# Kernel optimization log

Hardware: AMD Instinct MI355X
Metric: run time of the kernel (lower is better)

Reference implementation:

```python
import jax, jax.numpy as jnp
import numpy as np

N = 50000   # nodes
E = 800000  # edges
G = 64      # graphs in batch
D = 128     # joint_embed_dim
H = D // 2  # 64
NEG_SLOPE = 0.2


def _segment_softmax(logits, seg, n):
    m = jax.ops.segment_max(logits, seg, num_segments=n)
    m = jnp.where(jnp.isfinite(m), m, 0.0)
    e = jnp.exp(logits - m[seg])
    s = jax.ops.segment_sum(e, seg, num_segments=n)
    return e / (s[seg] + 1e-16)


def _gat_conv(x, src, dst, W, a_src, a_dst, b, n):
    # PyG GATConv, heads=1, add_self_loops=True
    loops = jnp.arange(n, dtype=src.dtype)
    s = jnp.concatenate([src, loops])
    d = jnp.concatenate([dst, loops])
    h = x @ W                                   # [n, out]
    alpha_s = h @ a_src                         # [n]
    alpha_d = h @ a_dst
    logit = jax.nn.leaky_relu(alpha_s[s] + alpha_d[d], NEG_SLOPE)  # [E+n]
    alpha = _segment_softmax(logit, d, n)
    out = jax.ops.segment_sum(h[s] * alpha[:, None], d, num_segments=n)
    return out + b


def _edge_conv(x, src, dst, We1, be1, We2, be2, n):
    # PyG EdgeConv: max_j nn(cat[x_i, x_j - x_i])
    xi = x[dst]
    xj = x[src]
    feats = jnp.concatenate([xi, xj - xi], axis=1)     # [E, 2*H]
    m = jax.nn.relu(feats @ We1 + be1)
    m = jax.nn.relu(m @ We2 + be2)
    out = jax.ops.segment_max(m, dst, num_segments=n)
    return jnp.where(jnp.isfinite(out), out, 0.0)


def setup_inputs() -> dict:
    key = jax.random.key(0)
    ks = jax.random.split(key, 24)
    x = jax.random.normal(ks[0], (N, 3), dtype=jnp.float32)
    edge_index = jax.random.randint(ks[1], (2, E), 0, N, dtype=jnp.int64)
    batch_ids = jnp.sort(jax.random.randint(ks[2], (N,), 0, G, dtype=jnp.int64))

    def w(k, shape, fan_in):
        return jax.random.normal(k, shape, dtype=jnp.float32) * (1.0 / np.sqrt(fan_in))

    inp = {
        "x": x, "edge_index": edge_index, "batch_ids": batch_ids,
        # GATConv1: 3 -> 64
        "W1": w(ks[3], (3, H), 3), "a1s": w(ks[4], (H,), H), "a1d": w(ks[5], (H,), H), "b1": jnp.zeros((H,), jnp.float32),
        # GATConv2: 64 -> 64
        "W2": w(ks[6], (H, H), H), "a2s": w(ks[7], (H,), H), "a2d": w(ks[8], (H,), H), "b2": jnp.zeros((H,), jnp.float32),
        # GATConv3: 128 -> 128
        "W3": w(ks[9], (D, D), D), "a3s": w(ks[10], (D,), D), "a3d": w(ks[11], (D,), D), "b3": jnp.zeros((D,), jnp.float32),
        # EdgeConv nn: 128 -> 128 -> 128
        "We1": w(ks[12], (D, D), D), "be1": jnp.zeros((D,), jnp.float32),
        "We2": w(ks[13], (D, D), D), "be2": jnp.zeros((D,), jnp.float32),
        # MLP: 256 -> 128 -> 128
        "Wm1": w(ks[14], (2 * D, D), 2 * D), "bm1": jnp.zeros((D,), jnp.float32),
        "Wm2": w(ks[15], (D, D), D), "bm2": jnp.zeros((D,), jnp.float32),
    }
    return inp


def reference(x, edge_index, batch_ids,
              W1, a1s, a1d, b1, W2, a2s, a2d, b2, W3, a3s, a3d, b3,
              We1, be1, We2, be2, Wm1, bm1, Wm2, bm2):
    src, dst = edge_index[0], edge_index[1]
    n = x.shape[0]
    # conv1 + relu (dropout is identity in eval)
    h = jax.nn.relu(_gat_conv(x, src, dst, W1, a1s, a1d, b1, n))
    # conv2 + elu
    h = jax.nn.elu(_gat_conv(h, src, dst, W2, a2s, a2d, b2, n))
    # edge_conv: 64 -> 128
    h = _edge_conv(h, src, dst, We1, be1, We2, be2, n)
    # conv3 + relu
    h = jax.nn.relu(_gat_conv(h, src, dst, W3, a3s, a3d, b3, n))
    # global mean / max pool over graphs
    sums = jax.ops.segment_sum(h, batch_ids, num_segments=G)
    cnts = jax.ops.segment_sum(jnp.ones((n, 1), h.dtype), batch_ids, num_segments=G)
    mean_pool = sums / jnp.maximum(cnts, 1.0)
    max_pool = jax.ops.segment_max(h, batch_ids, num_segments=G)
    max_pool = jnp.where(jnp.isfinite(max_pool), max_pool, 0.0)
    z = jnp.concatenate([mean_pool, max_pool], axis=1)    # [G, 256]
    z = jax.nn.relu(z @ Wm1 + bm1)
    z = jax.nn.relu(z @ Wm2 + bm2)
    norm = jnp.linalg.norm(z, axis=1, keepdims=True)
    return z / jnp.maximum(norm, 1e-12)
```

## Files before the change

### kernel.cpp

```cpp
#include <hip/hip_runtime.h>
#include <hip/hip_bf16.h>
#include <math.h>


typedef __attribute__((ext_vector_type(4))) float f32x4;
typedef __attribute__((ext_vector_type(8))) short bf16x8;
typedef __attribute__((ext_vector_type(8))) ushort u16x8;
typedef short s16x2 __attribute__((ext_vector_type(2)));

__device__ __forceinline__ float wave_sum(float v) {
#pragma unroll
  for (int o = 32; o > 0; o >>= 1) v += __shfl_xor(v, o, 64);
  return v;
}
__device__ __forceinline__ float wave_max(float v) {
#pragma unroll
  for (int o = 32; o > 0; o >>= 1) v = fmaxf(v, __shfl_xor(v, o, 64));
  return v;
}
__device__ __forceinline__ float half_sum(float v) {
#pragma unroll
  for (int o = 16; o > 0; o >>= 1) v += __shfl_xor(v, o, 64);
  return v;
}
__device__ __forceinline__ float half_max(float v) {
#pragma unroll
  for (int o = 16; o > 0; o >>= 1) v = fmaxf(v, __shfl_xor(v, o, 64));
  return v;
}
__device__ __forceinline__ float lrelu(float x) { return x >= 0.f ? x : 0.2f * x; }
__device__ __forceinline__ ushort f2bf(float f) {
  union { float f; unsigned u; } v; v.f = f;
  unsigned r = (v.u + 0x7fff + ((v.u >> 16) & 1)) >> 16;
  return (ushort)r;
}
__device__ __forceinline__ float bf2f(ushort u) {
  union { unsigned u; float f; } v; v.u = ((unsigned)u) << 16;
  return v.f;
}
__device__ __forceinline__ float bflo(unsigned v) { return __uint_as_float(v << 16); }
__device__ __forceinline__ float bfhi(unsigned v) { return __uint_as_float(v & 0xffff0000u); }
__device__ __forceinline__ unsigned pack2bf(float a, float b) {
  __hip_bfloat162 h = __float22bfloat162_rn(make_float2(a, b));
  union { __hip_bfloat162 h; unsigned u; } cv;
  cv.h = h;
  return cv.u;
}
__device__ __forceinline__ unsigned bfadd2_relu(unsigned a, unsigned b) {
  union { unsigned u; __hip_bfloat162 h; s16x2 s; } ua, ub, ur;
  ua.u = a;
  ub.u = b;
  ur.h = __hadd2(ua.h, ub.h);
  s16x2 z = (s16x2)0;
  ur.s = __builtin_elementwise_max(ur.s, z);
  return ur.u;
}


__global__ void count_kernel(const int* __restrict__ ei, int* __restrict__ deg, int E) {
  int e = blockIdx.x * 256 + threadIdx.x;
  if (e < E) atomicAdd(&deg[ei[E + e]], 1);
}

__global__ void scan_local(const int* __restrict__ deg, int* __restrict__ off,
                           int* __restrict__ bsum, int n) {
  __shared__ int buf[256];
  int i = blockIdx.x * 256 + threadIdx.x;
  int v = (i < n) ? deg[i] : 0;
  buf[threadIdx.x] = v;
  __syncthreads();
  int incl = v;
  for (int o = 1; o < 256; o <<= 1) {
    int t = (threadIdx.x >= o) ? buf[threadIdx.x - o] : 0;
    __syncthreads();
    incl += t;
    buf[threadIdx.x] = incl;
    __syncthreads();
  }
  if (i < n) off[i] = incl - v;
  if (threadIdx.x == 255) bsum[blockIdx.x] = incl;
}

__global__ void scan_bsum(int* __restrict__ bsum, int nb) {
  __shared__ int buf[256];
  int v = (threadIdx.x < nb) ? bsum[threadIdx.x] : 0;
  buf[threadIdx.x] = v;
  __syncthreads();
  int incl = v;
  for (int o = 1; o < 256; o <<= 1) {
    int t = (threadIdx.x >= o) ? buf[threadIdx.x - o] : 0;
    __syncthreads();
    incl += t;
    buf[threadIdx.x] = incl;
    __syncthreads();
  }
  if (threadIdx.x < nb) bsum[threadIdx.x] = incl - v;
}

__global__ void scan_add(int* __restrict__ off, const int* __restrict__ bsum, int n, int total) {
  int i = blockIdx.x * 256 + threadIdx.x;
  if (i < n) off[i] += bsum[blockIdx.x];
  if (i == 0) off[n] = total;
}

__global__ void scatter_kernel(const int* __restrict__ ei, const int* __restrict__ off,
                               int* __restrict__ cursor, int* __restrict__ csr_src,
                               int* __restrict__ csr_dst, int E) {
  int e = blockIdx.x * 256 + threadIdx.x;
  if (e < E) {
    int d = ei[E + e];
    int pos = off[d] + atomicAdd(&cursor[d], 1);
    csr_src[pos] = ei[e];
    csr_dst[pos] = d;
  }
}


template <int IN, int OUT>
__global__ __launch_bounds__(256) void node_linear_kernel(
    const float* __restrict__ x, const float* __restrict__ W,
    const float* __restrict__ av_s, const float* __restrict__ av_d,
    ushort* __restrict__ hb, float* __restrict__ as_out, float* __restrict__ ad_out, int n) {
  constexpr int NC = OUT / 64;
  constexpr int NB = 4;
  __shared__ float Wl[IN * OUT];
  if constexpr ((IN * OUT) % 1024 == 0) {
    for (int i = threadIdx.x; i < IN * OUT / 4; i += 256)
      ((float4*)Wl)[i] = ((const float4*)W)[i];
  } else {
    for (int i = threadIdx.x; i < IN * OUT; i += 256) Wl[i] = W[i];
  }
  __syncthreads();
  const int wid = threadIdx.x >> 6, lane = threadIdx.x & 63;
  const int n0 = (blockIdx.x * 4 + wid) * NB;
  if (n0 >= n) return;
  float acc[NB][NC];
#pragma unroll
  for (int j = 0; j < NB; ++j)
#pragma unroll
    for (int c = 0; c < NC; ++c) acc[j][c] = 0.f;
  int nidx[NB];
#pragma unroll
  for (int j = 0; j < NB; ++j) nidx[j] = min(n0 + j, n - 1);

  if constexpr ((IN & 3) == 0) {
#pragma unroll 2
    for (int k = 0; k < IN; k += 4) {
      float4 xv[NB];
#pragma unroll
      for (int j = 0; j < NB; ++j) xv[j] = *(const float4*)&x[nidx[j] * IN + k];
#pragma unroll
      for (int kk = 0; kk < 4; ++kk) {
        float w[NC];
        if constexpr (NC == 2) {
          float2 wv = *(const float2*)&Wl[(k + kk) * OUT + 2 * lane];
          w[0] = wv.x;
          w[1] = wv.y;
        } else {
          w[0] = Wl[(k + kk) * OUT + lane];
        }
#pragma unroll
        for (int j = 0; j < NB; ++j) {
          float xk = (kk == 0) ? xv[j].x : (kk == 1) ? xv[j].y : (kk == 2) ? xv[j].z : xv[j].w;
#pragma unroll
          for (int c = 0; c < NC; ++c) acc[j][c] += xk * w[c];
        }
      }
    }
  } else {
    for (int k = 0; k < IN; ++k) {
      float w[NC];
#pragma unroll
      for (int c = 0; c < NC; ++c) w[c] = (NC == 2) ? Wl[k * OUT + 2 * lane + c] : Wl[k * OUT + lane];
#pragma unroll
      for (int j = 0; j < NB; ++j) {
        float xk = x[nidx[j] * IN + k];
#pragma unroll
        for (int c = 0; c < NC; ++c) acc[j][c] += xk * w[c];
      }
    }
  }

  float a_sv[NC], a_dv[NC];
#pragma unroll
  for (int c = 0; c < NC; ++c) {
    const int col = (NC == 2) ? 2 * lane + c : lane;
    a_sv[c] = av_s[col];
    a_dv[c] = av_d[col];
  }
#pragma unroll
  for (int j = 0; j < NB; ++j) {
    int node = n0 + j;
    if (node >= n) break;
    float ps = 0.f, pd = 0.f;
#pragma unroll
    for (int c = 0; c < NC; ++c) {
      ps += acc[j][c] * a_sv[c];
      pd += acc[j][c] * a_dv[c];
    }
    if constexpr (NC == 2) {
      unsigned pk = pack2bf(acc[j][0], acc[j][1]);
      *(unsigned*)&hb[(size_t)node * OUT + 2 * lane] = pk;
    } else {
      hb[(size_t)node * OUT + lane] = f2bf(acc[j][0]);
    }
    ps = wave_sum(ps);
    pd = wave_sum(pd);
    if (lane == 0) {
      as_out[node] = ps;
      ad_out[node] = pd;
    }
  }
}


template <int K>
__global__ void compute_wa(const float* __restrict__ W, const float* __restrict__ a_s,
                           const float* __restrict__ a_d, float* __restrict__ wa_s,
                           float* __restrict__ wa_d) {
  const int k = threadIdx.x;
  float s = 0.f, d = 0.f;
  for (int j = 0; j < K; ++j) {
    const float w = W[k * K + j];
    s += w * a_s[j];
    d += w * a_d[j];
  }
  wa_s[k] = s;
  wa_d[k] = d;
}


#define NT 64
#define M1S 136
#define M2S 132

__global__ __launch_bounds__(256, 4) void node_mfma_kernel(
    const float* __restrict__ x, const ushort* __restrict__ Wcm,
    const float* __restrict__ wa_s, const float* __restrict__ wa_d,
    ushort* __restrict__ hb, float* __restrict__ as_out, float* __restrict__ ad_out, int n) {
  __shared__ __align__(16) char smem[NT * M2S * 4];
  __shared__ float swa[128], swd[128];
  ushort* m1 = (ushort*)smem;
  float* m2 = (float*)smem;
  const int tid = threadIdx.x;
  const int lane = tid & 63, wid = tid >> 6;
  const int quad = lane >> 4, l16 = lane & 15;
  const int row = tid >> 2, c0 = (tid & 3) * 32;

  bf16x8 bfrag[2][4];
#pragma unroll
  for (int ct = 0; ct < 2; ++ct) {
    const int nn = wid * 32 + ct * 16 + l16;
#pragma unroll
    for (int ks = 0; ks < 4; ++ks)
      bfrag[ct][ks] = *(const bf16x8*)&Wcm[nn * 128 + ks * 32 + quad * 8];
  }
  if (tid < 128) {
    swa[tid] = wa_s[tid];
    swd[tid] = wa_d[tid];
  }
  __syncthreads();

  const int n0 = blockIdx.x * NT;
  const int node = min(n0 + row, n - 1);

  float ps = 0.f, pd = 0.f;
  {
    const float4* xp = (const float4*)&x[(size_t)node * 128 + c0];
#pragma unroll
    for (int i = 0; i < 4; ++i) {
      const float4 a = xp[2 * i], b = xp[2 * i + 1];
      const float4 wa0 = *(const float4*)&swa[c0 + 8 * i];
      const float4 wa1 = *(const float4*)&swa[c0 + 8 * i + 4];
      const float4 wd0 = *(const float4*)&swd[c0 + 8 * i];
      const float4 wd1 = *(const float4*)&swd[c0 + 8 * i + 4];
      ps += a.x * wa0.x + a.y * wa0.y + a.z * wa0.z + a.w * wa0.w
          + b.x * wa1.x + b.y * wa1.y + b.z * wa1.z + b.w * wa1.w;
      pd += a.x * wd0.x + a.y * wd0.y + a.z * wd0.z + a.w * wd0.w
          + b.x * wd1.x + b.y * wd1.y + b.z * wd1.z + b.w * wd1.w;
      uint4 rr;
      rr.x = pack2bf(a.x, a.y);
      rr.y = pack2bf(a.z, a.w);
      rr.z = pack2bf(b.x, b.y);
      rr.w = pack2bf(b.z, b.w);
      *((uint4*)&m1[row * M1S + c0] + i) = rr;
    }
  }
  ps += __shfl_xor(ps, 1, 64);
  ps += __shfl_xor(ps, 2, 64);
  pd += __shfl_xor(pd, 1, 64);
  pd += __shfl_xor(pd, 2, 64);
  if ((tid & 3) == 0 && n0 + row < n) {
    as_out[n0 + row] = ps;
    ad_out[n0 + row] = pd;
  }
  __syncthreads();

  f32x4 acc[4][2];
#pragma unroll
  for (int rt = 0; rt < 4; ++rt)
#pragma unroll
    for (int ct = 0; ct < 2; ++ct) acc[rt][ct] = (f32x4)0.f;
#pragma unroll
  for (int ks = 0; ks < 4; ++ks) {
    bf16x8 afr[4];
#pragma unroll
    for (int rt = 0; rt < 4; ++rt)
      afr[rt] = *(const bf16x8*)&m1[(rt * 16 + l16) * M1S + ks * 32 + quad * 8];
#pragma unroll
    for (int rt = 0; rt < 4; ++rt)
#pragma unroll
      for (int ct = 0; ct < 2; ++ct)
        acc[rt][ct] = __builtin_amdgcn_mfma_f32_16x16x32_bf16(afr[rt], bfrag[ct][ks],
                                                              acc[rt][ct], 0, 0, 0);
  }
  __syncthreads();

#pragma unroll
  for (int ct = 0; ct < 2; ++ct) {
    const int col = wid * 32 + ct * 16 + l16;
#pragma unroll
    for (int rt = 0; rt < 4; ++rt)
#pragma unroll
      for (int r = 0; r < 4; ++r) {
        const int rr2 = rt * 16 + quad * 4 + r;
        m2[rr2 * M2S + col] = acc[rt][ct][r];
      }
  }
  __syncthreads();

  unsigned* hbu = (unsigned*)hb;
#pragma unroll
  for (int i = 0; i < 16; ++i) {
    const int r = wid + 4 * i;
    if (n0 + r < n)
      hbu[(size_t)(n0 + r) * 64 + lane] =
          pack2bf(m2[r * M2S + 2 * lane], m2[r * M2S + 2 * lane + 1]);
  }
}


#define M1S64 72
#define M2S64 68

__global__ __launch_bounds__(256, 4) void node_mfma64_kernel(
    const float* __restrict__ x, const ushort* __restrict__ Wcm,
    const float* __restrict__ wa_s, const float* __restrict__ wa_d,
    ushort* __restrict__ hb, float* __restrict__ as_out, float* __restrict__ ad_out, int n) {
  __shared__ __align__(16) char smem[NT * M2S64 * 4];
  __shared__ float swa[64], swd[64];
  ushort* m1 = (ushort*)smem;
  float* m2 = (float*)smem;
  const int tid = threadIdx.x;
  const int lane = tid & 63, wid = tid >> 6;
  const int quad = lane >> 4, l16 = lane & 15;
  const int row = tid >> 2, c0 = (tid & 3) * 16;

  bf16x8 bfrag[2];
#pragma unroll
  for (int ks = 0; ks < 2; ++ks)
    bfrag[ks] = *(const bf16x8*)&Wcm[(wid * 16 + l16) * 64 + ks * 32 + quad * 8];
  if (tid < 64) {
    swa[tid] = wa_s[tid];
    swd[tid] = wa_d[tid];
  }
  __syncthreads();

  const int n0 = blockIdx.x * NT;
  const int node = min(n0 + row, n - 1);

  float ps = 0.f, pd = 0.f;
  {
    const float4* xp = (const float4*)&x[(size_t)node * 64 + c0];
#pragma unroll
    for (int i = 0; i < 2; ++i) {
      const float4 a = xp[2 * i], b = xp[2 * i + 1];
      const float4 wa0 = *(const float4*)&swa[c0 + 8 * i];
      const float4 wa1 = *(const float4*)&swa[c0 + 8 * i + 4];
      const float4 wd0 = *(const float4*)&swd[c0 + 8 * i];
      const float4 wd1 = *(const float4*)&swd[c0 + 8 * i + 4];
      ps += a.x * wa0.x + a.y * wa0.y + a.z * wa0.z + a.w * wa0.w
          + b.x * wa1.x + b.y * wa1.y + b.z * wa1.z + b.w * wa1.w;
      pd += a.x * wd0.x + a.y * wd0.y + a.z * wd0.z + a.w * wd0.w
          + b.x * wd1.x + b.y * wd1.y + b.z * wd1.z + b.w * wd1.w;
      uint4 rr;
      rr.x = pack2bf(a.x, a.y);
      rr.y = pack2bf(a.z, a.w);
      rr.z = pack2bf(b.x, b.y);
      rr.w = pack2bf(b.z, b.w);
      *((uint4*)&m1[row * M1S64 + c0] + i) = rr;
    }
  }
  ps += __shfl_xor(ps, 1, 64);
  ps += __shfl_xor(ps, 2, 64);
  pd += __shfl_xor(pd, 1, 64);
  pd += __shfl_xor(pd, 2, 64);
  if ((tid & 3) == 0 && n0 + row < n) {
    as_out[n0 + row] = ps;
    ad_out[n0 + row] = pd;
  }
  __syncthreads();

  f32x4 acc[4];
#pragma unroll
  for (int rt = 0; rt < 4; ++rt) acc[rt] = (f32x4)0.f;
#pragma unroll
  for (int ks = 0; ks < 2; ++ks) {
    bf16x8 afr[4];
#pragma unroll
    for (int rt = 0; rt < 4; ++rt)
      afr[rt] = *(const bf16x8*)&m1[(rt * 16 + l16) * M1S64 + ks * 32 + quad * 8];
#pragma unroll
    for (int rt = 0; rt < 4; ++rt)
      acc[rt] = __builtin_amdgcn_mfma_f32_16x16x32_bf16(afr[rt], bfrag[ks], acc[rt], 0, 0, 0);
  }
  __syncthreads();

  {
    const int col = wid * 16 + l16;
#pragma unroll
    for (int rt = 0; rt < 4; ++rt)
#pragma unroll
      for (int r = 0; r < 4; ++r) {
        const int rr2 = rt * 16 + quad * 4 + r;
        m2[rr2 * M2S64 + col] = acc[rt][r];
      }
  }
  __syncthreads();

  unsigned* hbu = (unsigned*)hb;
#pragma unroll
  for (int i = 0; i < 8; ++i) {
    const int r = wid * 2 + (lane >> 5) + 8 * i;
    const int j = lane & 31;
    if (n0 + r < n)
      hbu[(size_t)(n0 + r) * 32 + j] =
          pack2bf(m2[r * M2S64 + 2 * j], m2[r * M2S64 + 2 * j + 1]);
  }
}


template <int OUT, int ACT>
__global__ __launch_bounds__(256) void gat_agg_kernel(
    const ushort* __restrict__ h, const float* __restrict__ as_, const float* __restrict__ ad_,
    const float* __restrict__ bias, const int* __restrict__ off, const int* __restrict__ csr_src,
    float* __restrict__ out, int n) {
  constexpr int NC = OUT / 64;
  __shared__ float wbuf[4][64];
  __shared__ int sbuf[4][64];
  const int wid = threadIdx.x >> 6, lane = threadIdx.x & 63;
  const int d = blockIdx.x * 4 + wid;
  if (d >= n) return;
  const int s0 = off[d], s1 = off[d + 1];
  const float ad = ad_[d];
  const float l_self = lrelu(as_[d] + ad);
  unsigned selfv = 0;
  ushort selfu = 0;
  if constexpr (NC == 2)
    selfv = *(const unsigned*)&h[(size_t)d * OUT + 2 * lane];
  else
    selfu = h[(size_t)d * OUT + lane];

  float m = l_self;
  float esum_l = 0.f;
  float acc[NC];
#pragma unroll
  for (int c = 0; c < NC; ++c) acc[c] = 0.f;

  for (int base = s0; base < s1; base += 64) {
    const int cnt = min(64, s1 - base);
    const int idx = base + lane;
    float l = -3.0e38f;
    int s_l = 0;
    if (idx < s1) {
      s_l = csr_src[idx];
      l = lrelu(as_[s_l] + ad);
    }
    const float cm = wave_max(l);
    if (cm > m) {
      const float alpha = __expf(m - cm);
      esum_l *= alpha;
#pragma unroll
      for (int c = 0; c < NC; ++c) acc[c] *= alpha;
      m = cm;
    }
    const float w_l = (idx < s1) ? __expf(l - m) : 0.f;
    sbuf[wid][lane] = s_l;
    wbuf[wid][lane] = w_l;
    esum_l += w_l;
    __threadfence_block();
    int j = 0;
    for (; j + 8 <= cnt; j += 8) {
      float w[8];
      int a[8];
#pragma unroll
      for (int t = 0; t < 8; ++t) {
        w[t] = wbuf[wid][j + t];
        a[t] = sbuf[wid][j + t];
      }
      if constexpr (NC == 2) {
        unsigned v[8];
#pragma unroll
        for (int t = 0; t < 8; ++t) v[t] = *(const unsigned*)&h[(size_t)a[t] * OUT + 2 * lane];
#pragma unroll
        for (int t = 0; t < 8; ++t) {
          acc[0] += w[t] * bflo(v[t]);
          acc[1] += w[t] * bfhi(v[t]);
        }
      } else {
        ushort v[8];
#pragma unroll
        for (int t = 0; t < 8; ++t) v[t] = h[(size_t)a[t] * OUT + lane];
#pragma unroll
        for (int t = 0; t < 8; ++t) acc[0] += w[t] * bf2f(v[t]);
      }
    }
    for (; j < cnt; ++j) {
      const float wj = wbuf[wid][j];
      const int aj = sbuf[wid][j];
      if constexpr (NC == 2) {
        const unsigned v = *(const unsigned*)&h[(size_t)aj * OUT + 2 * lane];
        acc[0] += wj * bflo(v);
        acc[1] += wj * bfhi(v);
      } else {
        acc[0] += wj * bf2f(h[(size_t)aj * OUT + lane]);
      }
    }
    __threadfence_block();
  }
  const float self_w = __expf(l_self - m);
  const float esum = wave_sum(esum_l) + self_w;
  if constexpr (NC == 2) {
    acc[0] += self_w * bflo(selfv);
    acc[1] += self_w * bfhi(selfv);
  } else {
    acc[0] += self_w * bf2f(selfu);
  }
  const float inv = 1.f / (esum + 1e-16f);
  if constexpr (NC == 2) {
    float2 o2;
    float v0 = acc[0] * inv + bias[2 * lane];
    float v1 = acc[1] * inv + bias[2 * lane + 1];
    if (ACT == 0) {
      v0 = fmaxf(v0, 0.f);
      v1 = fmaxf(v1, 0.f);
    } else {
      v0 = v0 > 0.f ? v0 : expm1f(v0);
      v1 = v1 > 0.f ? v1 : expm1f(v1);
    }
    o2.x = v0;
    o2.y = v1;
    *(float2*)&out[(size_t)d * OUT + 2 * lane] = o2;
  } else {
    float v = acc[0] * inv + bias[lane];
    if (ACT == 0)
      v = fmaxf(v, 0.f);
    else
      v = v > 0.f ? v : expm1f(v);
    out[(size_t)d * OUT + lane] = v;
  }
}


template <int ACT>
__global__ __launch_bounds__(256) void gat_agg64_kernel(
    const ushort* __restrict__ h, const float* __restrict__ as_, const float* __restrict__ ad_,
    const float* __restrict__ bias, const int* __restrict__ off, const int* __restrict__ csr_src,
    float* __restrict__ out, int n) {
  __shared__ float wbuf[4][64];
  __shared__ int sbuf[4][64];
  const int wid = threadIdx.x >> 6, lane = threadIdx.x & 63;
  const int half = lane >> 5, sl = lane & 31;
  const int d0 = blockIdx.x * 8 + wid * 2 + half;
  const bool wr = d0 < n;
  const int d = wr ? d0 : (n - 1);
  const int s0 = off[d], s1 = off[d + 1];
  const float ad = ad_[d];
  const float l_self = lrelu(as_[d] + ad);
  const unsigned selfv = *(const unsigned*)&h[(size_t)d * 64 + 2 * sl];

  float m = l_self;
  float esum_l = 0.f, acc0 = 0.f, acc1 = 0.f;

  for (int base = s0; base < s1; base += 32) {
    const int cnt = min(32, s1 - base);
    const int idx = base + sl;
    float l = -3.0e38f;
    int s_l = 0;
    if (idx < s1) {
      s_l = csr_src[idx];
      l = lrelu(as_[s_l] + ad);
    }
    const float cm = half_max(l);
    const float alpha = (cm > m) ? __expf(m - cm) : 1.f;
    esum_l *= alpha;
    acc0 *= alpha;
    acc1 *= alpha;
    m = fmaxf(m, cm);
    const float w_l = (idx < s1) ? __expf(l - m) : 0.f;
    sbuf[wid][half * 32 + sl] = s_l;
    wbuf[wid][half * 32 + sl] = w_l;
    esum_l += w_l;
    __threadfence_block();
    int j = 0;
    for (; j + 8 <= cnt; j += 8) {
      float w[8];
      int a[8];
#pragma unroll
      for (int t = 0; t < 8; ++t) {
        w[t] = wbuf[wid][half * 32 + j + t];
        a[t] = sbuf[wid][half * 32 + j + t];
      }
      unsigned v[8];
#pragma unroll
      for (int t = 0; t < 8; ++t) v[t] = *(const unsigned*)&h[(size_t)a[t] * 64 + 2 * sl];
#pragma unroll
      for (int t = 0; t < 8; ++t) {
        acc0 += w[t] * bflo(v[t]);
        acc1 += w[t] * bfhi(v[t]);
      }
    }
    for (; j < cnt; ++j) {
      const float wj = wbuf[wid][half * 32 + j];
      const int aj = sbuf[wid][half * 32 + j];
      const unsigned v = *(const unsigned*)&h[(size_t)aj * 64 + 2 * sl];
      acc0 += wj * bflo(v);
      acc1 += wj * bfhi(v);
    }
    __threadfence_block();
  }
  const float self_w = __expf(l_self - m);
  const float esum = half_sum(esum_l) + self_w;
  acc0 += self_w * bflo(selfv);
  acc1 += self_w * bfhi(selfv);
  const float inv = 1.f / (esum + 1e-16f);
  float v0 = acc0 * inv + bias[2 * sl];
  float v1 = acc1 * inv + bias[2 * sl + 1];
  if (ACT == 0) {
    v0 = fmaxf(v0, 0.f);
    v1 = fmaxf(v1, 0.f);
  } else {
    v0 = v0 > 0.f ? v0 : expm1f(v0);
    v1 = v1 > 0.f ? v1 : expm1f(v1);
  }
  if (wr) *(float2*)&out[(size_t)d * 64 + 2 * sl] = make_float2(v0, v1);
}


__global__ __launch_bounds__(256) void pq_kernel(
    const float* __restrict__ x, const float* __restrict__ We1, const float* __restrict__ be1,
    ushort* __restrict__ P, ushort* __restrict__ Q, int n) {
  __shared__ float AmB[64 * 128];
  __shared__ float Bm[64 * 128];
  for (int i = threadIdx.x; i < 64 * 128; i += 256) {
    float b = We1[64 * 128 + i];
    AmB[i] = We1[i] - b;
    Bm[i] = b;
  }
  __syncthreads();
  const int wid = threadIdx.x >> 6, lane = threadIdx.x & 63;
  const int n0 = (blockIdx.x * 4 + wid) * 4;
  if (n0 >= n) return;
  int nidx[4];
#pragma unroll
  for (int j = 0; j < 4; ++j) nidx[j] = min(n0 + j, n - 1);
  float ap[4][2], aq[4][2];
#pragma unroll
  for (int j = 0; j < 4; ++j) { ap[j][0] = ap[j][1] = aq[j][0] = aq[j][1] = 0.f; }
#pragma unroll 2
  for (int k = 0; k < 64; k += 4) {
    float4 xv[4];
#pragma unroll
    for (int j = 0; j < 4; ++j) xv[j] = *(const float4*)&x[nidx[j] * 64 + k];
#pragma unroll
    for (int kk = 0; kk < 4; ++kk) {
      const float wa0 = AmB[(k + kk) * 128 + lane], wa1 = AmB[(k + kk) * 128 + 64 + lane];
      const float wb0 = Bm[(k + kk) * 128 + lane], wb1 = Bm[(k + kk) * 128 + 64 + lane];
#pragma unroll
      for (int j = 0; j < 4; ++j) {
        const float xk = (kk == 0) ? xv[j].x : (kk == 1) ? xv[j].y : (kk == 2) ? xv[j].z : xv[j].w;
        ap[j][0] += xk * wa0;
        ap[j][1] += xk * wa1;
        aq[j][0] += xk * wb0;
        aq[j][1] += xk * wb1;
      }
    }
  }
  const float b0 = be1[lane], b1v = be1[64 + lane];
#pragma unroll
  for (int j = 0; j < 4; ++j) {
    const int node = n0 + j;
    if (node >= n) break;
    P[(size_t)node * 128 + lane] = f2bf(ap[j][0] + b0);
    P[(size_t)node * 128 + 64 + lane] = f2bf(ap[j][1] + b1v);
    Q[(size_t)node * 128 + lane] = f2bf(aq[j][0]);
    Q[(size_t)node * 128 + 64 + lane] = f2bf(aq[j][1]);
  }
}


template <int K>
__global__ void convert_wcm(const float* __restrict__ W, ushort* __restrict__ Wcm) {
  int i = blockIdx.x * 256 + threadIdx.x;
  if (i >= K * K) return;
  int k = i / K, nn = i % K;
  Wcm[nn * K + k] = f2bf(W[k * K + nn]);
}


#define TE 64
#define M2T 68

__global__ __launch_bounds__(256, 4) void edgeconv_mfma_kernel(
    const int* __restrict__ csr_src, const int* __restrict__ csr_dst,
    const ushort* __restrict__ P, const ushort* __restrict__ Q,
    const ushort* __restrict__ We2cm, const float* __restrict__ be2,
    float* __restrict__ out, int E, int ntiles) {
  __shared__ __align__(16) char smem[128 * M2T * 4];
  __shared__ __align__(16) int didx2[2][TE];
  ushort* m1 = (ushort*)smem;
  float* m2t = (float*)smem;
  const int tid = threadIdx.x;
  const int lane = tid & 63, wid = tid >> 6;
  const int quad = lane >> 4, l16 = lane & 15;
  const int row = tid >> 2;
  const int c0 = (tid & 3) * 32;

  bf16x8 bfrag[2][4];
#pragma unroll
  for (int ct = 0; ct < 2; ++ct) {
    const int nn = wid * 32 + ct * 16 + l16;
#pragma unroll
    for (int ks = 0; ks < 4; ++ks)
      bfrag[ct][ks] = *(const bf16x8*)&We2cm[nn * 128 + ks * 32 + quad * 8];
  }
  const float b0v = be2[wid * 32 + l16];
  const float b1v = be2[wid * 32 + 16 + l16];

  int t = blockIdx.x;
  if (t >= ntiles) return;

  uint4 pv[4], qv[4];
  {
    const int p = t * TE + row;
    int dd = 0, ss = 0;
    if (p < E) { dd = csr_dst[p]; ss = csr_src[p]; }
    const uint4* Pp = (const uint4*)&P[(size_t)dd * 128 + c0];
    const uint4* Qp = (const uint4*)&Q[(size_t)ss * 128 + c0];
#pragma unroll
    for (int i = 0; i < 4; ++i) { pv[i] = Pp[i]; qv[i] = Qp[i]; }
  }
  if (tid < TE) {
    const int p = t * TE + tid;
    didx2[0][tid] = (p < E) ? csr_dst[p] : -1;
  }

  int buf = 0;
  for (; t < ntiles; t += gridDim.x, buf ^= 1) {
    __syncthreads();

#pragma unroll
    for (int i = 0; i < 4; ++i) {
      uint4 rr;
      rr.x = bfadd2_relu(pv[i].x, qv[i].x);
      rr.y = bfadd2_relu(pv[i].y, qv[i].y);
      rr.z = bfadd2_relu(pv[i].z, qv[i].z);
      rr.w = bfadd2_relu(pv[i].w, qv[i].w);
      *((uint4*)&m1[row * M1S + c0] + i) = rr;
    }

    const int tn = t + gridDim.x;
    const bool hasNext = (tn < ntiles);
    int ddn = 0, ssn = 0;
    if (hasNext) {
      const int p = tn * TE + row;
      if (p < E) { ddn = csr_dst[p]; ssn = csr_src[p]; }
      if (tid < TE) {
        const int p2 = tn * TE + tid;
        didx2[buf ^ 1][tid] = (p2 < E) ? csr_dst[p2] : -1;
      }
    }
    __syncthreads();

    f32x4 acc[4][2];
#pragma unroll
    for (int rt = 0; rt < 4; ++rt)
#pragma unroll
      for (int ct = 0; ct < 2; ++ct) acc[rt][ct] = (f32x4)0.f;
#pragma unroll
    for (int ks = 0; ks < 4; ++ks) {
      bf16x8 afr[4];
#pragma unroll
      for (int rt = 0; rt < 4; ++rt)
        afr[rt] = *(const bf16x8*)&m1[(rt * 16 + l16) * M1S + ks * 32 + quad * 8];
#pragma unroll
      for (int rt = 0; rt < 4; ++rt)
#pragma unroll
        for (int ct = 0; ct < 2; ++ct)
          acc[rt][ct] = __builtin_amdgcn_mfma_f32_16x16x32_bf16(afr[rt], bfrag[ct][ks],
                                                                acc[rt][ct], 0, 0, 0);
    }

    if (hasNext) {
      const uint4* Pp = (const uint4*)&P[(size_t)ddn * 128 + c0];
      const uint4* Qp = (const uint4*)&Q[(size_t)ssn * 128 + c0];
#pragma unroll
      for (int i = 0; i < 4; ++i) { pv[i] = Pp[i]; qv[i] = Qp[i]; }
    }
    __syncthreads();

#pragma unroll
    for (int ct = 0; ct < 2; ++ct) {
      const int col = wid * 32 + ct * 16 + l16;
      const float b = ct == 0 ? b0v : b1v;
#pragma unroll
      for (int rt = 0; rt < 4; ++rt) {
        float4 mv;
        mv.x = fmaxf(acc[rt][ct][0] + b, 0.f);
        mv.y = fmaxf(acc[rt][ct][1] + b, 0.f);
        mv.z = fmaxf(acc[rt][ct][2] + b, 0.f);
        mv.w = fmaxf(acc[rt][ct][3] + b, 0.f);
        *(float4*)&m2t[col * M2T + rt * 16 + quad * 4] = mv;
      }
    }
    __syncthreads();

    const int col = tid & 127;
    const int r0 = (tid >> 7) * 32;
    float runmax = 0.f;
    int cur = -2;
#pragma unroll
    for (int i = 0; i < 8; ++i) {
      const int4 dv = *(const int4*)&didx2[buf][r0 + 4 * i];
      const float4 mv = *(const float4*)&m2t[col * M2T + r0 + 4 * i];
      const int da[4] = {dv.x, dv.y, dv.z, dv.w};
      const float ma[4] = {mv.x, mv.y, mv.z, mv.w};
#pragma unroll
      for (int r = 0; r < 4; ++r) {
        const int dd = da[r];
        if (dd != cur) {
          if (cur >= 0) atomicMax((int*)&out[(size_t)cur * 128 + col], __float_as_int(runmax));
          cur = dd;
          runmax = 0.f;
        }
        runmax = fmaxf(runmax, ma[r]);
      }
    }
    if (cur >= 0) atomicMax((int*)&out[(size_t)cur * 128 + col], __float_as_int(runmax));
  }
}


__global__ __launch_bounds__(256) void pool_part_kernel(
    const float* __restrict__ h, const int* __restrict__ bid,
    float* __restrict__ psum, float* __restrict__ pmax, int n) {
  const int chunk = (n + gridDim.x - 1) / gridDim.x;
  const int start = blockIdx.x * chunk;
  const int end = min(start + chunk, n);
  if (start >= end) return;
  const int c = threadIdx.x & 127, half = threadIdx.x >> 7;
  float sum = 0.f, mx = 0.f;
  int cur = -1;
  for (int i = start + half; i < end; i += 2) {
    const int g = bid[i];
    if (g != cur) {
      if (cur >= 0) {
        atomicAdd(&psum[cur * 128 + c], sum);
        atomicMax((int*)&pmax[cur * 128 + c], __float_as_int(mx));
      }
      cur = g;
      sum = 0.f;
      mx = 0.f;
    }
    const float v = h[(size_t)i * 128 + c];
    sum += v;
    mx = fmaxf(mx, v);
  }
  if (cur >= 0) {
    atomicAdd(&psum[cur * 128 + c], sum);
    atomicMax((int*)&pmax[cur * 128 + c], __float_as_int(mx));
  }
}


__global__ __launch_bounds__(128) void mlp_kernel(
    const float* __restrict__ psum, const float* __restrict__ pmax,
    const int* __restrict__ bid, int n,
    const float* __restrict__ Wm1, const float* __restrict__ bm1,
    const float* __restrict__ Wm2, const float* __restrict__ bm2,
    float* __restrict__ outp) {
  const int g = blockIdx.x;
  const int c = threadIdx.x;
  __shared__ float zin[256], z1[128];
  __shared__ int scnt;
  if (c == 0) {
    int lo = 0, hi = n;
    while (lo < hi) { int mid = (lo + hi) >> 1; if (bid[mid] < g) lo = mid + 1; else hi = mid; }
    const int start = lo;
    lo = start; hi = n;
    while (lo < hi) { int mid = (lo + hi) >> 1; if (bid[mid] < g + 1) lo = mid + 1; else hi = mid; }
    scnt = lo - start;
  }
  __syncthreads();
  const float invc = 1.f / fmaxf((float)scnt, 1.f);
  zin[c] = psum[g * 128 + c] * invc;
  zin[c + 128] = pmax[g * 128 + c];
  __syncthreads();
  float a = bm1[c];
  for (int k = 0; k < 256; ++k) a += zin[k] * Wm1[k * 128 + c];
  a = fmaxf(a, 0.f);
  z1[c] = a;
  __syncthreads();
  float b = bm2[c];
  for (int k = 0; k < 128; ++k) b += z1[k] * Wm2[k * 128 + c];
  b = fmaxf(b, 0.f);
  float ss = wave_sum(b * b);
  __shared__ float sred[2];
  if ((threadIdx.x & 63) == 0) sred[threadIdx.x >> 6] = ss;
  __syncthreads();
  const float nrm = sqrtf(sred[0] + sred[1]);
  outp[g * 128 + c] = b / fmaxf(nrm, 1e-12f);
}


extern "C" void kernel_launch(void* const* d_in, const int* in_sizes, int n_in, void* d_out,
                              int out_size, void* d_ws, size_t ws_size, hipStream_t stream) {
  const float* x = (const float*)d_in[0];
  const int* ei = (const int*)d_in[1];
  const int* bid = (const int*)d_in[2];
  const float* W1 = (const float*)d_in[3];
  const float* a1s = (const float*)d_in[4];
  const float* a1d = (const float*)d_in[5];
  const float* b1 = (const float*)d_in[6];
  const float* W2 = (const float*)d_in[7];
  const float* a2s = (const float*)d_in[8];
  const float* a2d = (const float*)d_in[9];
  const float* b2 = (const float*)d_in[10];
  const float* W3 = (const float*)d_in[11];
  const float* a3s = (const float*)d_in[12];
  const float* a3d = (const float*)d_in[13];
  const float* b3 = (const float*)d_in[14];
  const float* We1 = (const float*)d_in[15];
  const float* be1 = (const float*)d_in[16];
  const float* We2 = (const float*)d_in[17];
  const float* be2 = (const float*)d_in[18];
  const float* Wm1 = (const float*)d_in[19];
  const float* bm1 = (const float*)d_in[20];
  const float* Wm2 = (const float*)d_in[21];
  const float* bm2v = (const float*)d_in[22];

  const int n = in_sizes[0] / 3;
  const int E = in_sizes[1] / 2;
  const int G = out_size / 128;

  char* w = (char*)d_ws;
  size_t o = 0;
  auto alloc = [&](size_t bytes) {
    void* p = w + o;
    o = (o + bytes + 255) & ~(size_t)255;
    return p;
  };
  int* deg = (int*)alloc((size_t)n * 4);
  int* off = (int*)alloc((size_t)(n + 1) * 4);
  int* bsum = (int*)alloc(1024 * 4);
  int* csr_src = (int*)alloc((size_t)E * 4);
  int* csr_dst = (int*)alloc((size_t)E * 4);
  ushort* We2cm = (ushort*)alloc(128 * 128 * 2);
  ushort* W3cm = (ushort*)alloc(128 * 128 * 2);
  ushort* W2cm = (ushort*)alloc(64 * 64 * 2);
  float* was = (float*)alloc(128 * 4);
  float* wad = (float*)alloc(128 * 4);
  float* wa2s = (float*)alloc(64 * 4);
  float* wa2d = (float*)alloc(64 * 4);
  float* as_ = (float*)alloc((size_t)n * 4);
  float* ad_ = (float*)alloc((size_t)n * 4);
  ushort* T64 = (ushort*)alloc((size_t)n * 64 * 2);
  float* X64 = (float*)alloc((size_t)n * 64 * 4);
  ushort* Pbf = (ushort*)alloc((size_t)n * 128 * 2);
  ushort* Qbf = (ushort*)alloc((size_t)n * 128 * 2);
  float* H3 = (float*)alloc((size_t)n * 128 * 4);
  float* psum = (float*)alloc((size_t)G * 128 * 4);
  float* pmax = (float*)alloc((size_t)G * 128 * 4);
  (void)ws_size;

  ushort* Hbf = Pbf;
  float* C3out = H3;

  const int nb256 = (n + 255) / 256;
  const int ebl = (E + 255) / 256;
  const int nlb = (n + 15) / 16;
  const int agb = (n + 3) / 4;
  const int agb8 = (n + 7) / 8;
  const int ecb = (E + TE - 1) / TE;
  const int nmb = (n + NT - 1) / NT;

  hipMemsetAsync(deg, 0, (size_t)n * 4, stream);
  count_kernel<<<ebl, 256, 0, stream>>>(ei, deg, E);
  scan_local<<<nb256, 256, 0, stream>>>(deg, off, bsum, n);
  scan_bsum<<<1, 256, 0, stream>>>(bsum, nb256);
  scan_add<<<nb256, 256, 0, stream>>>(off, bsum, n, E);
  hipMemsetAsync(deg, 0, (size_t)n * 4, stream);
  scatter_kernel<<<ebl, 256, 0, stream>>>(ei, off, deg, csr_src, csr_dst, E);
  convert_wcm<128><<<64, 256, 0, stream>>>(We2, We2cm);
  convert_wcm<128><<<64, 256, 0, stream>>>(W3, W3cm);
  convert_wcm<64><<<16, 256, 0, stream>>>(W2, W2cm);
  compute_wa<128><<<1, 128, 0, stream>>>(W3, a3s, a3d, was, wad);
  compute_wa<64><<<1, 64, 0, stream>>>(W2, a2s, a2d, wa2s, wa2d);

  node_linear_kernel<3, 64><<<nlb, 256, 0, stream>>>(x, W1, a1s, a1d, T64, as_, ad_, n);
  gat_agg64_kernel<0><<<agb8, 256, 0, stream>>>(T64, as_, ad_, b1, off, csr_src, X64, n);
  node_mfma64_kernel<<<nmb, 256, 0, stream>>>(X64, W2cm, wa2s, wa2d, T64, as_, ad_, n);
  gat_agg64_kernel<1><<<agb8, 256, 0, stream>>>(T64, as_, ad_, b2, off, csr_src, X64, n);
  pq_kernel<<<nlb, 256, 0, stream>>>(X64, We1, be1, Pbf, Qbf, n);
  hipMemsetAsync(H3, 0, (size_t)n * 128 * 4, stream);
  edgeconv_mfma_kernel<<<1024, 256, 0, stream>>>(csr_src, csr_dst, Pbf, Qbf, We2cm, be2, H3,
                                                 E, ecb);
  node_mfma_kernel<<<nmb, 256, 0, stream>>>(H3, W3cm, was, wad, Hbf, as_, ad_, n);
  gat_agg_kernel<128, 0><<<agb, 256, 0, stream>>>(Hbf, as_, ad_, b3, off, csr_src, C3out, n);
  hipMemsetAsync(psum, 0, (size_t)G * 128 * 4 * 2, stream);
  pool_part_kernel<<<512, 256, 0, stream>>>(C3out, bid, psum, pmax, n);
  mlp_kernel<<<G, 128, 0, stream>>>(psum, pmax, bid, n, Wm1, bm1, Wm2, bm2v, (float*)d_out);
}
```

Baseline: 494.1 us.

## Use half-wave per node in conv3 aggregation and direct atomics in edgeconv

The 128-wide GAT aggregation now gives each destination node a 32-lane half-wave, with each lane handling four bf16 features through 8-byte loads. This doubles the nodes per block and makes the softmax rescale branch-free. The edgeconv kernel drops its shared-memory transpose and the two block barriers, issuing atomicMax straight from MFMA accumulator fragments with run-merging over four rows. The smaller LDS footprint allows higher occupancy (launch bound 5, 1280 blocks), but the atomic count may grow because runs are merged only within groups of four rows.

```diff
diff --git a/kernel.cpp b/kernel.cpp
--- a/kernel.cpp
+++ b/kernel.cpp
@@ -11,11 +11,6 @@
 __device__ __forceinline__ float wave_sum(float v) {
 #pragma unroll
   for (int o = 32; o > 0; o >>= 1) v += __shfl_xor(v, o, 64);
-  return v;
-}
-__device__ __forceinline__ float wave_max(float v) {
-#pragma unroll
-  for (int o = 32; o > 0; o >>= 1) v = fmaxf(v, __shfl_xor(v, o, 64));
   return v;
 }
 __device__ __forceinline__ float half_sum(float v) {
@@ -440,53 +435,46 @@
 }
 
 
-template <int OUT, int ACT>
-__global__ __launch_bounds__(256) void gat_agg_kernel(
+template <int ACT>
+__global__ __launch_bounds__(256) void gat_agg128h_kernel(
     const ushort* __restrict__ h, const float* __restrict__ as_, const float* __restrict__ ad_,
     const float* __restrict__ bias, const int* __restrict__ off, const int* __restrict__ csr_src,
     float* __restrict__ out, int n) {
-  constexpr int NC = OUT / 64;
   __shared__ float wbuf[4][64];
   __shared__ int sbuf[4][64];
   const int wid = threadIdx.x >> 6, lane = threadIdx.x & 63;
-  const int d = blockIdx.x * 4 + wid;
-  if (d >= n) return;
+  const int half = lane >> 5, sl = lane & 31;
+  const int d0 = blockIdx.x * 8 + wid * 2 + half;
+  const bool wr = d0 < n;
+  const int d = wr ? d0 : (n - 1);
   const int s0 = off[d], s1 = off[d + 1];
   const float ad = ad_[d];
   const float l_self = lrelu(as_[d] + ad);
-  unsigned selfv = 0;
-  ushort selfu = 0;
-  if constexpr (NC == 2)
-    selfv = *(const unsigned*)&h[(size_t)d * OUT + 2 * lane];
-  else
-    selfu = h[(size_t)d * OUT + lane];
+  const uint2 selfv = *(const uint2*)&h[(size_t)d * 128 + 4 * sl];
 
   float m = l_self;
-  float esum_l = 0.f;
-  float acc[NC];
-#pragma unroll
-  for (int c = 0; c < NC; ++c) acc[c] = 0.f;
-
-  for (int base = s0; base < s1; base += 64) {
-    const int cnt = min(64, s1 - base);
-    const int idx = base + lane;
+  float esum_l = 0.f, acc0 = 0.f, acc1 = 0.f, acc2 = 0.f, acc3 = 0.f;
+
+  for (int base = s0; base < s1; base += 32) {
+    const int cnt = min(32, s1 - base);
+    const int idx = base + sl;
     float l = -3.0e38f;
     int s_l = 0;
     if (idx < s1) {
       s_l = csr_src[idx];
       l = lrelu(as_[s_l] + ad);
     }
-    const float cm = wave_max(l);
-    if (cm > m) {
-      const float alpha = __expf(m - cm);
-      esum_l *= alpha;
-#pragma unroll
-      for (int c = 0; c < NC; ++c) acc[c] *= alpha;
-      m = cm;
-    }
+    const float cm = half_max(l);
+    const float alpha = (cm > m) ? __expf(m - cm) : 1.f;
+    esum_l *= alpha;
+    acc0 *= alpha;
+    acc1 *= alpha;
+    acc2 *= alpha;
+    acc3 *= alpha;
+    m = fmaxf(m, cm);
     const float w_l = (idx < s1) ? __expf(l - m) : 0.f;
-    sbuf[wid][lane] = s_l;
-    wbuf[wid][lane] = w_l;
+    sbuf[wid][half * 32 + sl] = s_l;
+    wbuf[wid][half * 32 + sl] = w_l;
     esum_l += w_l;
     __threadfence_block();
     int j = 0;
@@ -495,69 +483,60 @@
       int a[8];
 #pragma unroll
       for (int t = 0; t < 8; ++t) {
-        w[t] = wbuf[wid][j + t];
-        a[t] = sbuf[wid][j + t];
-      }
-      if constexpr (NC == 2) {
-        unsigned v[8];
-#pragma unroll
-        for (int t = 0; t < 8; ++t) v[t] = *(const unsigned*)&h[(size_t)a[t] * OUT + 2 * lane];
-#pragma unroll
-        for (int t = 0; t < 8; ++t) {
-          acc[0] += w[t] * bflo(v[t]);
-          acc[1] += w[t] * bfhi(v[t]);
-        }
-      } else {
-        ushort v[8];
-#pragma unroll
-        for (int t = 0; t < 8; ++t) v[t] = h[(size_t)a[t] * OUT + lane];
-#pragma unroll
-        for (int t = 0; t < 8; ++t) acc[0] += w[t] * bf2f(v[t]);
+        w[t] = wbuf[wid][half * 32 + j + t];
+        a[t] = sbuf[wid][half * 32 + j + t];
+      }
+      uint2 v[8];
+#pragma unroll
+      for (int t = 0; t < 8; ++t) v[t] = *(const uint2*)&h[(size_t)a[t] * 128 + 4 * sl];
+#pragma unroll
+      for (int t = 0; t < 8; ++t) {
+        acc0 += w[t] * bflo(v[t].x);
+        acc1 += w[t] * bfhi(v[t].x);
+        acc2 += w[t] * bflo(v[t].y);
+        acc3 += w[t] * bfhi(v[t].y);
       }
     }
     for (; j < cnt; ++j) {
-      const float wj = wbuf[wid][j];
-      const int aj = sbuf[wid][j];
-      if constexpr (NC == 2) {
-        const unsigned v = *(const unsigned*)&h[(size_t)aj * OUT + 2 * lane];
-        acc[0] += wj * bflo(v);
-        acc[1] += wj * bfhi(v);
-      } else {
-        acc[0] += wj * bf2f(h[(size_t)aj * OUT + lane]);
-      }
+      const float wj = wbuf[wid][half * 32 + j];
+      const int aj = sbuf[wid][half * 32 + j];
+      const uint2 v = *(const uint2*)&h[(size_t)aj * 128 + 4 * sl];
+      acc0 += wj * bflo(v.x);
+      acc1 += wj * bfhi(v.x);
+      acc2 += wj * bflo(v.y);
+      acc3 += wj * bfhi(v.y);
     }
     __threadfence_block();
   }
   const float self_w = __expf(l_self - m);
-  const float esum = wave_sum(esum_l) + self_w;
-  if constexpr (NC == 2) {
-    acc[0] += self_w * bflo(selfv);
-    acc[1] += self_w * bfhi(selfv);
+  const float esum = half_sum(esum_l) + self_w;
+  acc0 += self_w * bflo(selfv.x);
+  acc1 += self_w * bfhi(selfv.x);
+  acc2 += self_w * bflo(selfv.y);
+  acc3 += self_w * bfhi(selfv.y);
+  const float inv = 1.f / (esum + 1e-16f);
+  float v0 = acc0 * inv + bias[4 * sl];
+  float v1 = acc1 * inv + bias[4 * sl + 1];
+  float v2 = acc2 * inv + bias[4 * sl + 2];
+  float v3 = acc3 * inv + bias[4 * sl + 3];
+  if (ACT == 0) {
+    v0 = fmaxf(v0, 0.f);
+    v1 = fmaxf(v1, 0.f);
+    v2 = fmaxf(v2, 0.f);
+    v3 = fmaxf(v3, 0.f);
   } else {
-    acc[0] += self_w * bf2f(selfu);
-  }
-  const float inv = 1.f / (esum + 1e-16f);
-  if constexpr (NC == 2) {
-    float2 o2;
-    float v0 = acc[0] * inv + bias[2 * lane];
-    float v1 = acc[1] * inv + bias[2 * lane + 1];
-    if (ACT == 0) {
-      v0 = fmaxf(v0, 0.f);
-      v1 = fmaxf(v1, 0.f);
-    } else {
-      v0 = v0 > 0.f ? v0 : expm1f(v0);
-      v1 = v1 > 0.f ? v1 : expm1f(v1);
-    }
-    o2.x = v0;
-    o2.y = v1;
-    *(float2*)&out[(size_t)d * OUT + 2 * lane] = o2;
-  } else {
-    float v = acc[0] * inv + bias[lane];
-    if (ACT == 0)
-      v = fmaxf(v, 0.f);
-    else
-      v = v > 0.f ? v : expm1f(v);
-    out[(size_t)d * OUT + lane] = v;
+    v0 = v0 > 0.f ? v0 : expm1f(v0);
+    v1 = v1 > 0.f ? v1 : expm1f(v1);
+    v2 = v2 > 0.f ? v2 : expm1f(v2);
+    v3 = v3 > 0.f ? v3 : expm1f(v3);
+  }
+  if (wr) {
+    float4 o4;
+    o4.x = v0;
+    o4.y = v1;
+    o4.z = v2;
+    o4.w = v3;
+    *(float4*)&out[(size_t)d * 128 + 4 * sl] = o4;
   }
 }
 
@@ -709,17 +688,14 @@
 
 
 #define TE 64
-#define M2T 68
-
-__global__ __launch_bounds__(256, 4) void edgeconv_mfma_kernel(
+
+__global__ __launch_bounds__(256, 5) void edgeconv_mfma_kernel(
     const int* __restrict__ csr_src, const int* __restrict__ csr_dst,
     const ushort* __restrict__ P, const ushort* __restrict__ Q,
     const ushort* __restrict__ We2cm, const float* __restrict__ be2,
     float* __restrict__ out, int E, int ntiles) {
-  __shared__ __align__(16) char smem[128 * M2T * 4];
+  __shared__ __align__(16) ushort m1[TE * M1S];
   __shared__ __align__(16) int didx2[2][TE];
-  ushort* m1 = (ushort*)smem;
-  float* m2t = (float*)smem;
   const int tid = threadIdx.x;
   const int lane = tid & 63, wid = tid >> 6;
   const int quad = lane >> 4, l16 = lane & 15;
@@ -807,46 +783,32 @@
 #pragma unroll
       for (int i = 0; i < 4; ++i) { pv[i] = Pp[i]; qv[i] = Qp[i]; }
     }
-    __syncthreads();
-
-#pragma unroll
-    for (int ct = 0; ct < 2; ++ct) {
-      const int col = wid * 32 + ct * 16 + l16;
-      const float b = ct == 0 ? b0v : b1v;
-#pragma unroll
-      for (int rt = 0; rt < 4; ++rt) {
-        float4 mv;
-        mv.x = fmaxf(acc[rt][ct][0] + b, 0.f);
-        mv.y = fmaxf(acc[rt][ct][1] + b, 0.f);
-        mv.z = fmaxf(acc[rt][ct][2] + b, 0.f);
-        mv.w = fmaxf(acc[rt][ct][3] + b, 0.f);
-        *(float4*)&m2t[col * M2T + rt * 16 + quad * 4] = mv;
-      }
-    }
-    __syncthreads();
-
-    const int col = tid & 127;
-    const int r0 = (tid >> 7) * 32;
-    float runmax = 0.f;
-    int cur = -2;
-#pragma unroll
-    for (int i = 0; i < 8; ++i) {
-      const int4 dv = *(const int4*)&didx2[buf][r0 + 4 * i];
-      const float4 mv = *(const float4*)&m2t[col * M2T + r0 + 4 * i];
+
+#pragma unroll
+    for (int rt = 0; rt < 4; ++rt) {
+      const int4 dv = *(const int4*)&didx2[buf][rt * 16 + quad * 4];
       const int da[4] = {dv.x, dv.y, dv.z, dv.w};
-      const float ma[4] = {mv.x, mv.y, mv.z, mv.w};
-#pragma unroll
-      for (int r = 0; r < 4; ++r) {
-        const int dd = da[r];
-        if (dd != cur) {
-          if (cur >= 0) atomicMax((int*)&out[(size_t)cur * 128 + col], __float_as_int(runmax));
-          cur = dd;
-          runmax = 0.f;
+#pragma unroll
+      for (int ct = 0; ct < 2; ++ct) {
+        const int col = wid * 32 + ct * 16 + l16;
+        const float b = ct == 0 ? b0v : b1v;
+        float mx = fmaxf(acc[rt][ct][0] + b, 0.f);
+        int cur = da[0];
+#pragma unroll
+        for (int r = 1; r < 4; ++r) {
+          const float v = fmaxf(acc[rt][ct][r] + b, 0.f);
+          if (da[r] == cur) {
+            mx = fmaxf(mx, v);
+          } else {
+            if (cur >= 0)
+              atomicMax((int*)&out[(size_t)cur * 128 + col], __float_as_int(mx));
+            cur = da[r];
+            mx = v;
+          }
         }
-        runmax = fmaxf(runmax, ma[r]);
-      }
-    }
-    if (cur >= 0) atomicMax((int*)&out[(size_t)cur * 128 + col], __float_as_int(runmax));
+        if (cur >= 0) atomicMax((int*)&out[(size_t)cur * 128 + col], __float_as_int(mx));
+      }
+    }
   }
 }
 
@@ -989,7 +951,6 @@
   const int nb256 = (n + 255) / 256;
   const int ebl = (E + 255) / 256;
   const int nlb = (n + 15) / 16;
-  const int agb = (n + 3) / 4;
   const int agb8 = (n + 7) / 8;
   const int ecb = (E + TE - 1) / TE;
   const int nmb = (n + NT - 1) / NT;
@@ -1013,10 +974,10 @@
   gat_agg64_kernel<1><<<agb8, 256, 0, stream>>>(T64, as_, ad_, b2, off, csr_src, X64, n);
   pq_kernel<<<nlb, 256, 0, stream>>>(X64, We1, be1, Pbf, Qbf, n);
   hipMemsetAsync(H3, 0, (size_t)n * 128 * 4, stream);
-  edgeconv_mfma_kernel<<<1024, 256, 0, stream>>>(csr_src, csr_dst, Pbf, Qbf, We2cm, be2, H3,
+  edgeconv_mfma_kernel<<<1280, 256, 0, stream>>>(csr_src, csr_dst, Pbf, Qbf, We2cm, be2, H3,
                                                  E, ecb);
   node_mfma_kernel<<<nmb, 256, 0, stream>>>(H3, W3cm, was, wad, Hbf, as_, ad_, n);
-  gat_agg_kernel<128, 0><<<agb, 256, 0, stream>>>(Hbf, as_, ad_, b3, off, csr_src, C3out, n);
+  gat_agg128h_kernel<0><<<agb8, 256, 0, stream>>>(Hbf, as_, ad_, b3, off, csr_src, C3out, n);
   hipMemsetAsync(psum, 0, (size_t)G * 128 * 4 * 2, stream);
   pool_part_kernel<<<512, 256, 0, stream>>>(C3out, bid, psum, pmax, n);
   mlp_kernel<<<G, 128, 0, stream>>>(psum, pmax, bid, n, Wm1, bm1, Wm2, bm2v, (float*)d_out);
```

Result: slower. 685.2 us (+38.7%).
